# Kernel optimization log

Hardware: AMD Instinct MI355X
Metric: run time of the kernel (lower is better)

## Reference

```python
import jax, jax.numpy as jnp
import numpy as np

NEG_INF = -1e30  # stands in for torch's -inf diagonal mask; exp() underflows to 0 identically


def conv1x1(x, w, b):
    # x: [B,C,H,W], w: [O,C], b: [O]
    return jnp.einsum('oc,bchw->bohw', w, x) + b[None, :, None, None]


def s_module(x, qw, qb, kw, kb, vw, vb, gamma):
    # CCNet criss-cross attention with -inf diagonal masking on the H branch.
    B, C, H, W = x.shape
    q = conv1x1(x, qw, qb)  # [B,C8,H,W]
    k = conv1x1(x, kw, kb)  # [B,C8,H,W]
    v = conv1x1(x, vw, vb)  # [B,C,H,W]
    # energy_H[b,h,w,g] = <q[b,:,h,w], k[b,:,g,w]>  (attend along column)
    e_h = jnp.einsum('bchw,bcgw->bhwg', q, k)
    diag_mask = jnp.where(jnp.eye(H, dtype=bool), NEG_INF, 0.0).astype(x.dtype)
    e_h = e_h + diag_mask[None, :, None, :]  # mask h == g
    # energy_W[b,h,w,v] = <q[b,:,h,w], k[b,:,h,v]>  (attend along row)
    e_w = jnp.einsum('bchw,bchv->bhwv', q, k)
    att = jax.nn.softmax(jnp.concatenate([e_h, e_w], axis=-1), axis=-1)  # [B,H,W,H+W]
    a_h, a_w = att[..., :H], att[..., H:]
    out_h = jnp.einsum('bcgw,bhwg->bchw', v, a_h)
    out_w = jnp.einsum('bchv,bhwv->bchw', v, a_w)
    return gamma * (out_h + out_w) + x


def cam_module(x, fb, gamma):
    # channel attention: energy [B,C,C], max-sub trick, softmax, bmm back
    B, C, H, W = x.shape
    f = fb.reshape(B, C, H * W)
    energy = jnp.einsum('bcn,bdn->bcd', f, f)
    energy_new = jnp.max(energy, axis=-1, keepdims=True) - energy
    att = jax.nn.softmax(energy_new, axis=-1)
    out = jnp.einsum('bcd,bdn->bcn', att, f).reshape(B, C, H, W)
    return x + gamma * out


def _forward(x, fb, w_conv, b_conv, bn_g, bn_b,
             xq_w, xq_b, xk_w, xk_b, xv_w, xv_b, x_gamma,
             fq_w, fq_b, fk_w, fk_b, fv_w, fv_b, f_gamma,
             pam_gamma, pam_gamma2, cam_gamma):
    # MaxPool2d(kernel=2, stride=2)
    fbd = jax.lax.reduce_window(fb, -jnp.inf, jax.lax.max,
                                (1, 1, 2, 2), (1, 1, 2, 2), 'VALID')
    # convblock: 1x1 conv + BatchNorm (training-mode batch stats) + ReLU
    y = conv1x1(fbd, w_conv, b_conv)
    mu = jnp.mean(y, axis=(0, 2, 3), keepdims=True)
    var = jnp.var(y, axis=(0, 2, 3), keepdims=True)
    y = (y - mu) * jax.lax.rsqrt(var + 1e-5)
    y = y * bn_g[None, :, None, None] + bn_b[None, :, None, None]
    y = jax.nn.relu(y)
    # FeedbackSpatialAttention (PAM)
    x_att = pam_gamma * s_module(x, xq_w, xq_b, xk_w, xk_b, xv_w, xv_b, x_gamma)
    fb_att = s_module(y, fq_w, fq_b, fk_w, fk_b, fv_w, fv_b, f_gamma)
    pam_out = x + x_att + pam_gamma2 * fb_att
    # CAM on (x, processed fb)
    cam_out = cam_module(x, y, cam_gamma)
    return pam_out + cam_out


def setup_inputs() -> dict:
    key = jax.random.key(0)
    ks = jax.random.split(key, 24)
    B, C, H, W = 4, 64, 128, 128
    C8 = C // 8
    d = {
        'x': jax.random.normal(ks[0], (B, C, H, W), jnp.float32),
        'fb': jax.random.normal(ks[1], (B, C, 2 * H, 2 * W), jnp.float32),
        'w_conv': jax.random.normal(ks[2], (C, C), jnp.float32) * 0.05,
        'b_conv': jax.random.normal(ks[3], (C,), jnp.float32) * 0.02,
        'bn_g': jax.random.uniform(ks[4], (C,), jnp.float32, 0.5, 1.5),
        'bn_b': jax.random.normal(ks[5], (C,), jnp.float32) * 0.02,
        'xq_w': jax.random.normal(ks[6], (C8, C), jnp.float32) * 0.05,
        'xq_b': jax.random.normal(ks[7], (C8,), jnp.float32) * 0.02,
        'xk_w': jax.random.normal(ks[8], (C8, C), jnp.float32) * 0.05,
        'xk_b': jax.random.normal(ks[9], (C8,), jnp.float32) * 0.02,
        'xv_w': jax.random.normal(ks[10], (C, C), jnp.float32) * 0.05,
        'xv_b': jax.random.normal(ks[11], (C,), jnp.float32) * 0.02,
        'x_gamma': jax.random.normal(ks[12], (1,), jnp.float32) * 0.1,
        'fq_w': jax.random.normal(ks[13], (C8, C), jnp.float32) * 0.05,
        'fq_b': jax.random.normal(ks[14], (C8,), jnp.float32) * 0.02,
        'fk_w': jax.random.normal(ks[15], (C8, C), jnp.float32) * 0.05,
        'fk_b': jax.random.normal(ks[16], (C8,), jnp.float32) * 0.02,
        'fv_w': jax.random.normal(ks[17], (C, C), jnp.float32) * 0.05,
        'fv_b': jax.random.normal(ks[18], (C,), jnp.float32) * 0.02,
        'f_gamma': jax.random.normal(ks[19], (1,), jnp.float32) * 0.1,
        'pam_gamma': jax.random.normal(ks[20], (1,), jnp.float32) * 0.1,
        'pam_gamma2': jax.random.normal(ks[21], (1,), jnp.float32) * 0.1,
        'cam_gamma': jax.random.normal(ks[22], (1,), jnp.float32) * 0.1,
    }
    return d


def reference(x, fb, w_conv, b_conv, bn_g, bn_b,
              xq_w, xq_b, xk_w, xk_b, xv_w, xv_b, x_gamma,
              fq_w, fq_b, fk_w, fk_b, fv_w, fv_b, f_gamma,
              pam_gamma, pam_gamma2, cam_gamma):
    return _forward(x, fb, w_conv, b_conv, bn_g, bn_b,
                    xq_w, xq_b, xk_w, xk_b, xv_w, xv_b, x_gamma,
                    fq_w, fq_b, fk_w, fk_b, fv_w, fv_b, f_gamma,
                    pam_gamma, pam_gamma2, cam_gamma)
```

## Files before the change

### kernel.cpp

```cpp
#include <hip/hip_runtime.h>
#include <hip/hip_bf16.h>

#define NP 16384
#define NB 4

typedef __hip_bfloat16 bf16;
typedef unsigned short u16;
typedef unsigned short us8 __attribute__((ext_vector_type(8)));
typedef unsigned short us4 __attribute__((ext_vector_type(4)));
typedef short ss8 __attribute__((ext_vector_type(8)));
typedef float f32x4 __attribute__((ext_vector_type(4)));
__device__ __forceinline__ float bf2f(const bf16 v) { return __bfloat162float(v); }
__device__ __forceinline__ bf16 f2bf(float v) { return __float2bfloat16(v); }
__device__ __forceinline__ float bfu(u16 h) {
  return __uint_as_float(((unsigned)h) << 16);
}
__device__ __forceinline__ u16 fbu(float v) {
  bf16 b = f2bf(v);
  return *(u16*)&b;
}


__global__ __launch_bounds__(256) void k_pool_conv(
    const float* __restrict__ fb, const float* __restrict__ wconv,
    const float* __restrict__ bconv, bf16* __restrict__ Y) {
  __shared__ float wS[64 * 65], bS[64], Xs[4096];
  int tid = threadIdx.x;
  int b = blockIdx.x >> 8, tile = blockIdx.x & 255;
  int n0 = tile * 64;
  for (int i = tid; i < 4096; i += 256) wS[(i >> 6) * 65 + (i & 63)] = wconv[i];
  if (tid < 64) bS[tid] = bconv[tid];
  for (int i = tid; i < 4096; i += 256) {
    int c = i >> 6, px = i & 63;
    int n = n0 + px, h = n >> 7, w = n & 127;
    size_t fbase = ((size_t)((b * 64 + c) * 256 + 2 * h)) * 256 + 2 * w;
    float2 v01 = *(const float2*)(fb + fbase);
    float2 v23 = *(const float2*)(fb + fbase + 256);
    Xs[i] = fmaxf(fmaxf(v01.x, v01.y), fmaxf(v23.x, v23.y));
  }
  __syncthreads();
  int ty = tid >> 4, tx = tid & 15;
  float acc[4][4];
#pragma unroll
  for (int i = 0; i < 4; ++i) {
    float bv = bS[ty + 16 * i];
#pragma unroll
    for (int j = 0; j < 4; ++j) acc[i][j] = bv;
  }
  for (int c = 0; c < 64; ++c) {
    float xv[4], wv[4];
#pragma unroll
    for (int j = 0; j < 4; ++j) xv[j] = Xs[c * 64 + tx * 4 + j];
#pragma unroll
    for (int i = 0; i < 4; ++i) wv[i] = wS[(ty + 16 * i) * 65 + c];
#pragma unroll
    for (int i = 0; i < 4; ++i)
#pragma unroll
      for (int j = 0; j < 4; ++j) acc[i][j] = fmaf(wv[i], xv[j], acc[i][j]);
  }
#pragma unroll
  for (int i = 0; i < 4; ++i) {
    int ch = ty + 16 * i;
    bf16* yb = Y + (size_t)(b * 64 + ch) * NP + n0 + tx * 4;
#pragma unroll
    for (int j = 0; j < 4; ++j) yb[j] = f2bf(acc[i][j]);
  }
}

__global__ __launch_bounds__(256) void k_stats_p1(const bf16* __restrict__ Y,
                                                  float* __restrict__ PS) {
  int blk = blockIdx.x, tid = threadIdx.x;
  int o = blk >> 3, slab = blk & 7;
  int b = slab >> 1, half = slab & 1;
  const us8* vp =
      (const us8*)(Y + ((size_t)(b * 64 + o)) * NP + half * 8192);
  float s = 0.f, ss = 0.f;
#pragma unroll
  for (int it = 0; it < 4; ++it) {
    us8 v = vp[tid + 256 * it];
#pragma unroll
    for (int e = 0; e < 8; ++e) {
      float f = bfu(v[e]);
      s += f;
      ss = fmaf(f, f, ss);
    }
  }
  for (int off = 32; off > 0; off >>= 1) {
    s += __shfl_down(s, off, 64);
    ss += __shfl_down(ss, off, 64);
  }
  __shared__ float sh[8];
  int wv = tid >> 6, ln = tid & 63;
  if (ln == 0) { sh[wv] = s; sh[4 + wv] = ss; }
  __syncthreads();
  if (tid == 0) {
    PS[blk] = sh[0] + sh[1] + sh[2] + sh[3];
    PS[512 + blk] = sh[4] + sh[5] + sh[6] + sh[7];
  }
}

__global__ __launch_bounds__(64) void k_stats_p2(
    const float* __restrict__ PS, const float* __restrict__ bng,
    const float* __restrict__ bnb, float* __restrict__ SCALE,
    float* __restrict__ SHIFT, const float* xg, const float* fg,
    const float* pg, const float* pg2, const float* cg,
    float* __restrict__ HDR) {
  int o = threadIdx.x;
  float s = 0.f, ss = 0.f;
#pragma unroll
  for (int k = 0; k < 8; ++k) {
    s += PS[o * 8 + k];
    ss += PS[512 + o * 8 + k];
  }
  const float inv = 1.0f / (NB * NP);
  float mu = s * inv;
  float var = ss * inv - mu * mu;
  float r = rsqrtf(var + 1e-5f);
  float sc = r * bng[o];
  SCALE[o] = sc;
  SHIFT[o] = bnb[o] - mu * sc;
  if (o == 0) {
    float vpg = pg[0];
    HDR[1] = vpg * xg[0];
    HDR[2] = pg2[0] * fg[0];
    HDR[3] = 2.0f + vpg;
    HDR[4] = pg2[0];
    HDR[5] = cg[0];
  }
}

__global__ __launch_bounds__(256, 4) void k_conv_mfma(
    const float* __restrict__ xin, const bf16* __restrict__ Yin,
    const float* __restrict__ SCALE, const float* __restrict__ SHIFT,
    const float* __restrict__ qw0, const float* __restrict__ qb0,
    const float* __restrict__ kw0, const float* __restrict__ kb0,
    const float* __restrict__ vw0, const float* __restrict__ vb0,
    const float* __restrict__ qw1, const float* __restrict__ qb1,
    const float* __restrict__ kw1, const float* __restrict__ kb1,
    const float* __restrict__ vw1, const float* __restrict__ vb1,
    bf16* __restrict__ QK, bf16* __restrict__ V) {
  __shared__ __align__(16) u16 Xs[128 * 64];
  __shared__ __align__(16) u16 wHi[80 * 64], wLo[80 * 64];
  __shared__ float bS[80];
  int tid = threadIdx.x;
  int m = blockIdx.x >> 9;
  int b = (blockIdx.x >> 7) & 3;
  int tile = blockIdx.x & 127;
  int n0 = tile * 128;
  const float* qw = m ? qw1 : qw0;
  const float* qb = m ? qb1 : qb0;
  const float* kw = m ? kw1 : kw0;
  const float* kb = m ? kb1 : kb0;
  const float* vw = m ? vw1 : vw0;
  const float* vb = m ? vb1 : vb0;
  for (int i = tid; i < 5120; i += 256) {
    int oc = i >> 6, c = i & 63;
    float w;
    if (oc < 8) w = qw[oc * 64 + c];
    else if (oc < 16) w = kw[(oc - 8) * 64 + c];
    else w = vw[(oc - 16) * 64 + c];
    u16 hb = fbu(w);
    u16 lb = fbu(w - bfu(hb));
    int idx = (oc * 64 + c) ^ ((oc & 7) << 3);
    wHi[idx] = hb;
    wLo[idx] = lb;
  }
  if (tid < 80)
    bS[tid] = (tid < 8) ? qb[tid] : (tid < 16) ? kb[tid - 8] : vb[tid - 16];
  if (m) {
    for (int i2 = tid; i2 < 1024; i2 += 256) {
      int c = i2 >> 4, vj = i2 & 15;
      us8 v = *(const us8*)(Yin + (size_t)(b * 64 + c) * NP + n0 + vj * 8);
      float sc = SCALE[c], sh = SHIFT[c];
#pragma unroll
      for (int e = 0; e < 8; ++e) {
        int px = vj * 8 + e;
        float f = fmaxf(fmaf(bfu(v[e]), sc, sh), 0.f);
        Xs[(px * 64 + c) ^ ((((px & 7) ^ ((px >> 3) & 7))) << 3)] = fbu(f);
      }
    }
  } else {
    for (int i2 = tid; i2 < 2048; i2 += 256) {
      int c = i2 >> 5, vj = i2 & 31;
      float4 v = *(const float4*)(xin + (size_t)(b * 64 + c) * NP + n0 + vj * 4);
      float vv[4] = {v.x, v.y, v.z, v.w};
#pragma unroll
      for (int r = 0; r < 4; ++r) {
        int px = vj * 4 + r;
        Xs[(px * 64 + c) ^ ((((px & 7) ^ ((px >> 3) & 7))) << 3)] = fbu(vv[r]);
      }
    }
  }
  __syncthreads();
  int lane = tid & 63, wv = tid >> 6;
  int il = lane & 15, gq = lane >> 4;
  int pxb = wv * 32;
  ss8 afr[2][2];
#pragma unroll
  for (int sub = 0; sub < 2; ++sub)
#pragma unroll
    for (int ks = 0; ks < 2; ++ks) {
      int px = pxb + sub * 16 + il;
      int idx =
          (px * 64 + ks * 32 + gq * 8) ^ ((((px & 7) ^ ((px >> 3) & 7))) << 3);
      afr[sub][ks] = *(const ss8*)&Xs[idx];
    }
#pragma unroll
  for (int oct = 0; oct < 5; ++oct) {
    int oc = oct * 16 + il;
    ss8 wh[2], wl[2];
#pragma unroll
    for (int ks = 0; ks < 2; ++ks) {
      int idx = (oc * 64 + ks * 32 + gq * 8) ^ ((oc & 7) << 3);
      wh[ks] = *(const ss8*)&wHi[idx];
      wl[ks] = *(const ss8*)&wLo[idx];
    }
    float bv = bS[oc];
    bf16* dst;
    size_t basep;
    if (oc < 8) { dst = QK; basep = (size_t)(((m * 2 + 0) * 4 + b) * 8 + oc) * NP; }
    else if (oc < 16) { dst = QK; basep = (size_t)(((m * 2 + 1) * 4 + b) * 8 + (oc - 8)) * NP; }
    else { dst = V; basep = (size_t)((m * 4 + b) * 64 + (oc - 16)) * NP; }
#pragma unroll
    for (int sub = 0; sub < 2; ++sub) {
      f32x4 acc = {bv, bv, bv, bv};
#pragma unroll
      for (int ks = 0; ks < 2; ++ks) {
        acc = __builtin_amdgcn_mfma_f32_16x16x32_bf16(afr[sub][ks], wh[ks], acc, 0, 0, 0);
        acc = __builtin_amdgcn_mfma_f32_16x16x32_bf16(afr[sub][ks], wl[ks], acc, 0, 0, 0);
      }
      int px0 = pxb + sub * 16 + gq * 4;
      us4 ov;
#pragma unroll
      for (int r = 0; r < 4; ++r) ov[r] = fbu(acc[r]);
      *(us4*)(dst + basep + n0 + px0) = ov;
    }
  }
}

__global__ __launch_bounds__(256) void k_transpose2(
    const u16* __restrict__ inA, u16* __restrict__ outA,
    const u16* __restrict__ inB, u16* __restrict__ outB, int nA) {
  int tileId = blockIdx.x & 15;
  int plane = blockIdx.x >> 4;
  const u16* ip;
  u16* op;
  if (plane < nA) {
    ip = inA + (size_t)plane * NP;
    op = outA + (size_t)plane * NP;
  } else {
    ip = inB + (size_t)(plane - nA) * NP;
    op = outB + (size_t)(plane - nA) * NP;
  }
  int th = tileId >> 2, tw = tileId & 3;
  __shared__ u16 t[32][33];
  int lx = threadIdx.x & 31, ly = threadIdx.x >> 5;
  for (int i = 0; i < 32; i += 8)
    t[ly + i][lx] = ip[(size_t)(th * 32 + ly + i) * 128 + tw * 32 + lx];
  __syncthreads();
  for (int i = 0; i < 32; i += 8)
    op[(size_t)(tw * 32 + ly + i) * 128 + th * 32 + lx] = t[lx][ly + i];
}

__global__ __launch_bounds__(256, 4) void k_av(
    const bf16* __restrict__ QK, const bf16* __restrict__ QKT,
    const bf16* __restrict__ V, const bf16* __restrict__ VT,
    float* __restrict__ MWp, float* __restrict__ LWp,
    float* __restrict__ MHp, float* __restrict__ LHp,
    float* __restrict__ OW, bf16* __restrict__ OHT) {
  int blk = blockIdx.x;
  int m = blk & 1, mode = (blk >> 1) & 1;
  int bid = blk >> 2;
  int b = bid >> 7, h = bid & 127;
  const bf16* qkbase = mode ? QKT : QK;
  const bf16* Qp = qkbase + (size_t)(((m * 2 + 0) * 4 + b) * 8) * NP;
  const bf16* Kp = qkbase + (size_t)(((m * 2 + 1) * 4 + b) * 8) * NP;
  const bf16* Vp = (mode ? VT : V) + (size_t)((m * 4 + b) * 64) * NP;
  __shared__ __align__(16) u16 qT[128 * 8];
  __shared__ __align__(16) u16 kT[128 * 8];
  __shared__ __align__(16) u16 Vs[64 * 136];
  int tid = threadIdx.x;
  {
    int c = (tid >> 4) & 7, vj = tid & 15;
    const bf16* src = (tid < 128) ? Qp : Kp;
    u16* dst = (tid < 128) ? qT : kT;
    const us8* sp = (const us8*)(src + (size_t)c * NP + (size_t)h * 128);
    us8 sv = sp[vj];
#pragma unroll
    for (int e = 0; e < 8; ++e) {
      int j = vj * 8 + e;
      int p = ((j & 7) << 4) | (j >> 3);
      dst[p * 8 + c] = sv[e];
    }
  }
  for (int i2 = tid; i2 < 1024; i2 += 256) {
    int c = i2 >> 4, vj = i2 & 15;
    const us8* vp = (const us8*)(Vp + (size_t)c * NP + (size_t)h * 128);
    us8 vv = vp[vj];
    *(us8*)&Vs[c * 136 + vj * 8] = vv;
  }
  __syncthreads();
  int lane = tid & 63, wv = tid >> 6;
  int il = lane & 15, gq = lane >> 4;
  size_t sb = (size_t)(m * 4 + b) * NP;
  float* owBase = OW + (size_t)((m * 4 + b) * 64) * NP + (size_t)h * 128;
  bf16* ohBase = OHT + (size_t)((m * 4 + b) * 64) * NP + (size_t)h * 128;
#pragma unroll
  for (int sub = 0; sub < 2; ++sub) {
    int ib = wv * 32 + sub * 16;
    int i = ib + il;
    int pi = ((i & 7) << 4) | (i >> 3);
    us8 qv = *(const us8*)&qT[pi * 8];
    float qr[8];
#pragma unroll
    for (int c = 0; c < 8; ++c) qr[c] = bfu(qv[c]);
    float scr[4][8];
    float mrow = -3.0e38f;
#pragma unroll
    for (int ks = 0; ks < 4; ++ks) {
#pragma unroll
      for (int e = 0; e < 8; ++e) {
        int j = ks * 32 + gq * 8 + e;
        int pj = ((j & 7) << 4) | (j >> 3);
        us8 kv = *(const us8*)&kT[pj * 8];
        float s = 0.f;
#pragma unroll
        for (int c = 0; c < 8; ++c) s = fmaf(qr[c], bfu(kv[c]), s);
        if (mode && j == i) s = -1.0e30f;
        scr[ks][e] = s;
        mrow = fmaxf(mrow, s);
      }
    }
    mrow = fmaxf(mrow, __shfl_xor(mrow, 16, 64));
    mrow = fmaxf(mrow, __shfl_xor(mrow, 32, 64));
    float l = 0.f;
    ss8 afr[4];
#pragma unroll
    for (int ks = 0; ks < 4; ++ks) {
      ss8 af;
#pragma unroll
      for (int e = 0; e < 8; ++e) {
        float ev = __expf(scr[ks][e] - mrow);
        l += ev;
        af[e] = (short)fbu(ev);
      }
      afr[ks] = af;
    }
    l += __shfl_xor(l, 16, 64);
    l += __shfl_xor(l, 32, 64);
    if (gq == 0) {
      if (mode == 0) {
        MWp[sb + (size_t)h * 128 + i] = mrow;
        LWp[sb + (size_t)h * 128 + i] = l;
      } else {
        MHp[sb + (size_t)i * 128 + h] = mrow;
        LHp[sb + (size_t)i * 128 + h] = l;
      }
    }
#pragma unroll
    for (int ct = 0; ct < 4; ++ct) {
      f32x4 acc = {0.f, 0.f, 0.f, 0.f};
#pragma unroll
      for (int ks = 0; ks < 4; ++ks) {
        ss8 bv = *(const ss8*)&Vs[(ct * 16 + il) * 136 + ks * 32 + gq * 8];
        acc = __builtin_amdgcn_mfma_f32_16x16x32_bf16(afr[ks], bv, acc, 0, 0, 0);
      }
      int cch = ct * 16 + il;
      int i0 = ib + gq * 4;
      if (mode == 0) {
#pragma unroll
        for (int r = 0; r < 4; ++r)
          owBase[(size_t)cch * NP + (size_t)(i0 + r)] = acc[r];
      } else {
#pragma unroll
        for (int r = 0; r < 4; ++r)
          ohBase[(size_t)cch * NP + (size_t)(i0 + r)] = f2bf(acc[r]);
      }
    }
  }
}

__global__ __launch_bounds__(256) void k_merge2(
    const bf16* __restrict__ OHT, const float* __restrict__ OW,
    const float* __restrict__ MWp, const float* __restrict__ LWp,
    const float* __restrict__ MHp, const float* __restrict__ LHp,
    const float* __restrict__ HDR, float* __restrict__ ACC) {
  int tileId = blockIdx.x & 15;
  int plane = blockIdx.x >> 4;
  int b = plane >> 6;
  int th = tileId >> 2, tw = tileId & 3;
  __shared__ float t0[32][33], t1[32][33];
  int lx = threadIdx.x & 31, ly = threadIdx.x >> 5;
  const bf16* ip0 = OHT + (size_t)plane * NP;
  const bf16* ip1 = OHT + (size_t)(256 + plane) * NP;
  for (int i = 0; i < 32; i += 8) {
    size_t idx = (size_t)(th * 32 + ly + i) * 128 + tw * 32 + lx;
    t0[ly + i][lx] = bf2f(ip0[idx]);
    t1[ly + i][lx] = bf2f(ip1[idx]);
  }
  __syncthreads();
  float sc0 = HDR[1], sc1 = HDR[2];
  float* op = ACC + (size_t)plane * NP;
  const float* ow0 = OW + (size_t)plane * NP;
  const float* ow1 = OW + (size_t)(256 + plane) * NP;
  size_t s0 = (size_t)b * NP, s1 = (size_t)(4 + b) * NP;
  for (int i = 0; i < 32; i += 8) {
    int hh = tw * 32 + ly + i, ww = th * 32 + lx;
    size_t idx = (size_t)hh * 128 + ww;
    float mw0 = MWp[s0 + idx], mh0 = MHp[s0 + idx];
    float M0 = fmaxf(mw0, mh0);
    float ea0 = __expf(mw0 - M0), eb0 = __expf(mh0 - M0);
    float inv0 = 1.0f / (LWp[s0 + idx] * ea0 + LHp[s0 + idx] * eb0);
    float v0 = (ea0 * ow0[idx] + eb0 * t0[lx][ly + i]) * inv0;
    float mw1 = MWp[s1 + idx], mh1 = MHp[s1 + idx];
    float M1 = fmaxf(mw1, mh1);
    float ea1 = __expf(mw1 - M1), eb1 = __expf(mh1 - M1);
    float inv1 = 1.0f / (LWp[s1 + idx] * ea1 + LHp[s1 + idx] * eb1);
    float v1 = (ea1 * ow1[idx] + eb1 * t1[lx][ly + i]) * inv1;
    op[idx] = sc0 * v0 + sc1 * v1;
  }
}

__global__ __launch_bounds__(256) void k_gram(const bf16* __restrict__ Y,
                                              const float* __restrict__ SCALE,
                                              const float* __restrict__ SHIFT,
                                              float* __restrict__ GP) {
  int b = blockIdx.x >> 7, ch = (blockIdx.x >> 2) & 31, t = blockIdx.x & 3;
  int tid = threadIdx.x;
  __shared__ float fs[64 * 129];
  int cg = tid >> 4, dg = tid & 15;
  float acc[4][4];
#pragma unroll
  for (int i = 0; i < 4; ++i)
#pragma unroll
    for (int jx = 0; jx < 4; ++jx) acc[i][jx] = 0.f;
  const bf16* yb = Y + (size_t)b * 64 * NP + ch * 512;
  for (int idx = tid; idx < 8192; idx += 256) {
    int c = idx >> 7, j = idx & 127;
    float v = fmaf(bf2f(yb[(size_t)c * NP + t * 128 + j]), SCALE[c], SHIFT[c]);
    fs[c * 129 + j] = fmaxf(v, 0.f);
  }
  __syncthreads();
  for (int j = 0; j < 128; ++j) {
    float a[4], d[4];
#pragma unroll
    for (int i = 0; i < 4; ++i) a[i] = fs[(cg * 4 + i) * 129 + j];
#pragma unroll
    for (int i = 0; i < 4; ++i) d[i] = fs[(dg * 4 + i) * 129 + j];
#pragma unroll
    for (int i = 0; i < 4; ++i)
#pragma unroll
      for (int jx = 0; jx < 4; ++jx) acc[i][jx] = fmaf(a[i], d[jx], acc[i][jx]);
  }
  float* gp = GP + ((size_t)(b * 128) + ch * 4 + t) * 4096;
#pragma unroll
  for (int i = 0; i < 4; ++i)
#pragma unroll
    for (int jx = 0; jx < 4; ++jx)
      gp[(cg * 4 + i) * 64 + dg * 4 + jx] = acc[i][jx];
}

__global__ __launch_bounds__(256) void k_gram_reduce(const float* __restrict__ GP,
                                                     float* __restrict__ CATT) {
  int b = blockIdx.x >> 4, rg = blockIdx.x & 15;
  int tid = threadIdx.x;
  __shared__ float Es[256];
  int e = rg * 256 + tid;
  float s = 0.f;
  for (int k = 0; k < 128; ++k) s += GP[((size_t)b * 128 + k) * 4096 + e];
  Es[tid] = s;
  __syncthreads();
  int wv = tid >> 6, ln = tid & 63;
  float v = Es[wv * 64 + ln];
  float mn = v;
  for (int off = 32; off; off >>= 1) mn = fminf(mn, __shfl_xor(mn, off, 64));
  float ev = __expf(mn - v);
  float ssum = ev;
  for (int off = 32; off; off >>= 1) ssum += __shfl_xor(ssum, off, 64);
  CATT[((size_t)b * 64 + rg * 4 + wv) * 64 + ln] = ev / ssum;
}

__global__ __launch_bounds__(256) void k_final(
    const float* __restrict__ x, const bf16* __restrict__ Y,
    const float* __restrict__ SCALE, const float* __restrict__ SHIFT,
    const float* __restrict__ CATT, const float* __restrict__ HDR,
    float* __restrict__ OUT) {
  __shared__ float attS[64 * 65], Ys[64 * 65];
  int tid = threadIdx.x;
  int b = blockIdx.x >> 8, tile = blockIdx.x & 255;
  int n0 = tile * 64;
  for (int i = tid; i < 4096; i += 256)
    attS[(i >> 6) * 65 + (i & 63)] = CATT[(size_t)b * 4096 + i];
  for (int i = tid; i < 4096; i += 256) {
    int d = i >> 6, px = i & 63;
    float v = fmaf(bf2f(Y[(size_t)(b * 64 + d) * NP + n0 + px]), SCALE[d], SHIFT[d]);
    Ys[d * 65 + px] = fmaxf(v, 0.f);
  }
  __syncthreads();
  int cg = tid >> 4, pgx = tid & 15;
  int c0 = cg * 4, p0 = pgx * 4;
  float acc[4][4];
#pragma unroll
  for (int i = 0; i < 4; ++i)
#pragma unroll
    for (int j = 0; j < 4; ++j) acc[i][j] = 0.f;
  for (int d = 0; d < 64; ++d) {
    float a[4], yv[4];
#pragma unroll
    for (int i = 0; i < 4; ++i) a[i] = attS[(c0 + i) * 65 + d];
#pragma unroll
    for (int j = 0; j < 4; ++j) yv[j] = Ys[d * 65 + p0 + j];
#pragma unroll
    for (int i = 0; i < 4; ++i)
#pragma unroll
      for (int j = 0; j < 4; ++j) acc[i][j] = fmaf(a[i], yv[j], acc[i][j]);
  }
  float c2pg = HDR[3], fpg2 = HDR[4], fcg = HDR[5];
#pragma unroll
  for (int i = 0; i < 4; ++i) {
    size_t base = (size_t)(b * 64 + c0 + i) * NP + n0 + p0;
#pragma unroll
    for (int j = 0; j < 4; ++j) {
      float yv = Ys[(c0 + i) * 65 + p0 + j];
      OUT[base + j] =
          c2pg * x[base + j] + fpg2 * yv + OUT[base + j] + fcg * acc[i][j];
    }
  }
}

extern "C" void kernel_launch(void* const* d_in, const int* in_sizes, int n_in,
                              void* d_out, int out_size, void* d_ws, size_t ws_size,
                              hipStream_t stream) {
  const float* x = (const float*)d_in[0];
  const float* fbp = (const float*)d_in[1];

  char* base = (char*)d_ws;
  float* HDR = (float*)base;
  float* SCALE = HDR + 16;
  float* SHIFT = SCALE + 64;
  char* p = base + 4096;
  bf16* Y = (bf16*)p;    p += 8388608;
  bf16* QK = (bf16*)p;   p += 4194304;
  bf16* QKT = (bf16*)p;  p += 4194304;
  bf16* V = (bf16*)p;    p += 16777216;
  bf16* VT = (bf16*)p;   p += 16777216;
  float* MWp = (float*)p; p += 524288;
  float* LWp = (float*)p; p += 524288;
  float* MHp = (float*)p; p += 524288;
  float* LHp = (float*)p; p += 524288;
  bf16* OHT = (bf16*)p;  p += 16777216;
  float* OW = (float*)p; p += 33554432;
  float* GP = (float*)p; p += 8388608;
  float* CATT = (float*)p; p += 1048576;
  float* ACC = (float*)d_out;
  float* PS = (float*)QK;

  k_pool_conv<<<1024, 256, 0, stream>>>(fbp, (const float*)d_in[2],
                                        (const float*)d_in[3], Y);
  k_stats_p1<<<512, 256, 0, stream>>>(Y, PS);
  k_stats_p2<<<1, 64, 0, stream>>>(PS, (const float*)d_in[4],
                                   (const float*)d_in[5], SCALE, SHIFT,
                                   (const float*)d_in[12], (const float*)d_in[19],
                                   (const float*)d_in[20], (const float*)d_in[21],
                                   (const float*)d_in[22], HDR);

  k_conv_mfma<<<1024, 256, 0, stream>>>(
      x, Y, SCALE, SHIFT,
      (const float*)d_in[6], (const float*)d_in[7], (const float*)d_in[8],
      (const float*)d_in[9], (const float*)d_in[10], (const float*)d_in[11],
      (const float*)d_in[13], (const float*)d_in[14], (const float*)d_in[15],
      (const float*)d_in[16], (const float*)d_in[17], (const float*)d_in[18],
      QK, V);
  k_transpose2<<<10240, 256, 0, stream>>>((const u16*)QK, (u16*)QKT,
                                          (const u16*)V, (u16*)VT, 128);
  k_av<<<2048, 256, 0, stream>>>(QK, QKT, V, VT, MWp, LWp, MHp, LHp, OW, OHT);
  k_merge2<<<4096, 256, 0, stream>>>(OHT, OW, MWp, LWp, MHp, LHp, HDR, ACC);

  k_gram<<<512, 256, 0, stream>>>(Y, SCALE, SHIFT, GP);
  k_gram_reduce<<<64, 256, 0, stream>>>(GP, CATT);
  k_final<<<1024, 256, 0, stream>>>(x, Y, SCALE, SHIFT, CATT, HDR,
                                    (float*)d_out);
}
```

Measured before the change: 282.8 us.

## Use bf16 MFMA with split-weight precision for pool+conv kernel

Rewrites the pooled 1x1 conv kernel to compute with 16x16x32 bf16 MFMA instructions instead of scalar FP32 FMAs. Weights are split into hi/lo bf16 parts to keep precision, activations are rounded to bf16, and LDS uses XOR swizzling. Pooling loads become float4 and outputs are written as 4-wide vectors. It also adds an occupancy hint. The trade-off is rounding the pooled activations to bf16, which loses some accuracy.

```diff
diff --git a/kernel.cpp b/kernel.cpp
--- a/kernel.cpp
+++ b/kernel.cpp
@@ -21,49 +21,73 @@
 }
 
 
-__global__ __launch_bounds__(256) void k_pool_conv(
+__global__ __launch_bounds__(256, 4) void k_pool_conv(
     const float* __restrict__ fb, const float* __restrict__ wconv,
     const float* __restrict__ bconv, bf16* __restrict__ Y) {
-  __shared__ float wS[64 * 65], bS[64], Xs[4096];
+  __shared__ __align__(16) u16 Xs[64 * 64];
+  __shared__ __align__(16) u16 wHi[64 * 64], wLo[64 * 64];
+  __shared__ float bS[64];
   int tid = threadIdx.x;
   int b = blockIdx.x >> 8, tile = blockIdx.x & 255;
   int n0 = tile * 64;
-  for (int i = tid; i < 4096; i += 256) wS[(i >> 6) * 65 + (i & 63)] = wconv[i];
+  int h = n0 >> 7, w0 = n0 & 127;
+  for (int i = tid; i < 4096; i += 256) {
+    int oc = i >> 6, c = i & 63;
+    float wv = wconv[oc * 64 + c];
+    u16 hb = fbu(wv);
+    u16 lb = fbu(wv - bfu(hb));
+    int idx = i ^ ((oc & 7) << 3);
+    wHi[idx] = hb;
+    wLo[idx] = lb;
+  }
   if (tid < 64) bS[tid] = bconv[tid];
-  for (int i = tid; i < 4096; i += 256) {
-    int c = i >> 6, px = i & 63;
-    int n = n0 + px, h = n >> 7, w = n & 127;
-    size_t fbase = ((size_t)((b * 64 + c) * 256 + 2 * h)) * 256 + 2 * w;
-    float2 v01 = *(const float2*)(fb + fbase);
-    float2 v23 = *(const float2*)(fb + fbase + 256);
-    Xs[i] = fmaxf(fmaxf(v01.x, v01.y), fmaxf(v23.x, v23.y));
-  }
-  __syncthreads();
-  int ty = tid >> 4, tx = tid & 15;
-  float acc[4][4];
-#pragma unroll
-  for (int i = 0; i < 4; ++i) {
-    float bv = bS[ty + 16 * i];
-#pragma unroll
-    for (int j = 0; j < 4; ++j) acc[i][j] = bv;
-  }
-  for (int c = 0; c < 64; ++c) {
-    float xv[4], wv[4];
-#pragma unroll
-    for (int j = 0; j < 4; ++j) xv[j] = Xs[c * 64 + tx * 4 + j];
-#pragma unroll
-    for (int i = 0; i < 4; ++i) wv[i] = wS[(ty + 16 * i) * 65 + c];
-#pragma unroll
-    for (int i = 0; i < 4; ++i)
-#pragma unroll
-      for (int j = 0; j < 4; ++j) acc[i][j] = fmaf(wv[i], xv[j], acc[i][j]);
-  }
-#pragma unroll
-  for (int i = 0; i < 4; ++i) {
-    int ch = ty + 16 * i;
-    bf16* yb = Y + (size_t)(b * 64 + ch) * NP + n0 + tx * 4;
-#pragma unroll
-    for (int j = 0; j < 4; ++j) yb[j] = f2bf(acc[i][j]);
+  for (int i2 = tid; i2 < 2048; i2 += 256) {
+    int c = i2 >> 5, pp = i2 & 31;
+    const float* r0 =
+        fb + ((size_t)((b * 64 + c) * 256 + 2 * h)) * 256 + 2 * w0 + 4 * pp;
+    float4 v0 = *(const float4*)r0;
+    float4 v1 = *(const float4*)(r0 + 256);
+    int px = 2 * pp;
+    float a0 = fmaxf(fmaxf(v0.x, v0.y), fmaxf(v1.x, v1.y));
+    float a1 = fmaxf(fmaxf(v0.z, v0.w), fmaxf(v1.z, v1.w));
+    Xs[(px * 64 + c) ^ ((((px & 7) ^ ((px >> 3) & 7))) << 3)] = fbu(a0);
+    px++;
+    Xs[(px * 64 + c) ^ ((((px & 7) ^ ((px >> 3) & 7))) << 3)] = fbu(a1);
+  }
+  __syncthreads();
+  int lane = tid & 63, wv = tid >> 6;
+  int il = lane & 15, gq = lane >> 4;
+  int pxb = wv * 16;
+  ss8 afr[2];
+#pragma unroll
+  for (int ks = 0; ks < 2; ++ks) {
+    int px = pxb + il;
+    int idx =
+        (px * 64 + ks * 32 + gq * 8) ^ ((((px & 7) ^ ((px >> 3) & 7))) << 3);
+    afr[ks] = *(const ss8*)&Xs[idx];
+  }
+#pragma unroll
+  for (int oct = 0; oct < 4; ++oct) {
+    int oc = oct * 16 + il;
+    ss8 wh[2], wl[2];
+#pragma unroll
+    for (int ks = 0; ks < 2; ++ks) {
+      int idx = (oc * 64 + ks * 32 + gq * 8) ^ ((oc & 7) << 3);
+      wh[ks] = *(const ss8*)&wHi[idx];
+      wl[ks] = *(const ss8*)&wLo[idx];
+    }
+    float bv = bS[oc];
+    f32x4 acc = {bv, bv, bv, bv};
+#pragma unroll
+    for (int ks = 0; ks < 2; ++ks) {
+      acc = __builtin_amdgcn_mfma_f32_16x16x32_bf16(afr[ks], wh[ks], acc, 0, 0, 0);
+      acc = __builtin_amdgcn_mfma_f32_16x16x32_bf16(afr[ks], wl[ks], acc, 0, 0, 0);
+    }
+    int px0 = pxb + gq * 4;
+    us4 ov;
+#pragma unroll
+    for (int r = 0; r < 4; ++r) ov[r] = fbu(acc[r]);
+    *(us4*)(Y + (size_t)(b * 64 + oc) * NP + n0 + px0) = ov;
   }
 }
 
```

New measurement: 277.4 us. About the same (-1.9%).
